# Optimization experiments

Measured on AMD Instinct MI355X. Metric: run time of the kernel, lower is better.

Reference implementation:

```python
import jax, jax.numpy as jnp
import numpy as np
import math

B, S, D, H, P = 4, 2048, 512, 8, 64
HD = D // H


def setup_inputs() -> dict:
    key = jax.random.key(0)
    ks = jax.random.split(key, 12)
    inp = {
        "query": jax.random.normal(ks[0], (B, S, D), jnp.float32),
        "key": jax.random.normal(ks[1], (B, S, D), jnp.float32),
        "value": jax.random.normal(ks[2], (B, S, D), jnp.float32),
        "query_pos_em": jax.random.normal(ks[3], (B, S, P), jnp.float32),
        "key_pos_em": jax.random.normal(ks[4], (B, S, P), jnp.float32),
        "mask": jax.random.randint(ks[5], (B, S), 0, 2, jnp.int32),
        # learned params (bias=False linears, LayerNorm affine)
        "Wq": jax.random.normal(ks[6], (D, D), jnp.float32) / math.sqrt(D),
        "Wk": jax.random.normal(ks[7], (D, D), jnp.float32) / math.sqrt(D),
        "Wv": jax.random.normal(ks[8], (D, D), jnp.float32) / math.sqrt(D),
        "Wo": jax.random.normal(ks[9], (D, D), jnp.float32) / math.sqrt(D),
        "ln_gamma": jnp.ones((D,), jnp.float32),
        "ln_beta": jnp.zeros((D,), jnp.float32),
    }
    return inp


def _split_heads(x):
    # (B,S,D) -> (B,H,S,HD)
    return x.reshape(B, S, H, HD).transpose(0, 2, 1, 3)


def reference(query, key, value, query_pos_em, key_pos_em, mask,
              Wq, Wk, Wv, Wo, ln_gamma, ln_beta):
    residual = query
    q = _split_heads(query @ Wq)
    k = _split_heads(key @ Wk)
    v = _split_heads(value @ Wv)

    # positional similarity: softmax over (B,S,S)
    simi = jax.nn.softmax(jnp.einsum('bqp,bkp->bqk', query_pos_em, key_pos_em), axis=-1)

    # scaled dot-product modulated elementwise by similarity (broadcast over heads)
    prod = jnp.einsum('bhqd,bhkd->bhqk', q, k) / math.sqrt(HD)
    prod = prod * simi[:, None, :, :]

    # additive mask: (mask-1)*1e8, broadcast [:, None, None, :]
    m = (mask.astype(prod.dtype) - 1.0) * 1e8
    prod = prod + m[:, None, None, :]

    attn = jax.nn.softmax(prod, axis=-1)
    out = jnp.einsum('bhqk,bhkd->bhqd', attn, v)  # (B,H,S,HD)
    out = out.transpose(0, 2, 1, 3).reshape(B, S, D)
    out = out @ Wo  # dropout is identity in eval mode

    x = residual + out
    mu = jnp.mean(x, axis=-1, keepdims=True)
    var = jnp.var(x, axis=-1, keepdims=True)
    return (x - mu) / jnp.sqrt(var + 1e-5) * ln_gamma + ln_beta
```

## Files before the change

kernel.cpp:

```cpp
#include <hip/hip_runtime.h>
#include <hip/hip_bf16.h>

#define Bq 4
#define Sq 2048
#define Dq 512
#define Hq 8
#define HDq 64
#define Pq 64

typedef __attribute__((ext_vector_type(8))) short short8;
typedef __attribute__((ext_vector_type(4))) float f32x4;

__device__ inline unsigned short f2bf(float f) {
  unsigned int u = __float_as_uint(f);
  unsigned int r = u + 0x7FFFu + ((u >> 16) & 1u);
  return (unsigned short)(r >> 16);
}
__device__ inline float bf2f(unsigned short s) {
  return __uint_as_float(((unsigned int)s) << 16);
}
__device__ inline short8 ld8f(const float* __restrict__ p) {
  const float4 a = *(const float4*)p;
  const float4 b = *(const float4*)(p + 4);
  short8 r;
  r[0] = (short)f2bf(a.x); r[1] = (short)f2bf(a.y); r[2] = (short)f2bf(a.z); r[3] = (short)f2bf(a.w);
  r[4] = (short)f2bf(b.x); r[5] = (short)f2bf(b.y); r[6] = (short)f2bf(b.z); r[7] = (short)f2bf(b.w);
  return r;
}

__global__ __launch_bounds__(256) void prep(const float* __restrict__ qpe,
                                            const float* __restrict__ kpe,
                                            const int* __restrict__ mask,
                                            unsigned short* __restrict__ qpeb,
                                            unsigned short* __restrict__ kpeb,
                                            float* __restrict__ mb) {
  const int bid = blockIdx.x;
  if (bid < 256) {
    int i = bid * 256 + threadIdx.x;
    *(short8*)&qpeb[(size_t)i * 8] = ld8f(qpe + (size_t)i * 8);
  } else if (bid < 512) {
    int i = (bid - 256) * 256 + threadIdx.x;
    *(short8*)&kpeb[(size_t)i * 8] = ld8f(kpe + (size_t)i * 8);
  } else {
    int i = (bid - 512) * 256 + threadIdx.x;
    mb[i] = ((float)mask[i] - 1.0f) * 1.442695041e8f;
  }
}

__global__ __launch_bounds__(256) void convW4(const float* __restrict__ Wq,
                                              const float* __restrict__ Wk,
                                              const float* __restrict__ Wv,
                                              const float* __restrict__ Wo,
                                              unsigned short* __restrict__ Wqt,
                                              unsigned short* __restrict__ Wkt,
                                              unsigned short* __restrict__ Wvt,
                                              unsigned short* __restrict__ Wot) {
  __shared__ float tile[32][33];
  const int z = blockIdx.z;
  const float* W = z == 0 ? Wq : z == 1 ? Wk : z == 2 ? Wv : Wo;
  unsigned short* Wt = z == 0 ? Wqt : z == 1 ? Wkt : z == 2 ? Wvt : Wot;
  const float scale = (z == 0) ? 0.125f : 1.0f;
  const int tx = threadIdx.x & 31, ty = threadIdx.x >> 5;
  const int n0 = blockIdx.x * 32, k0 = blockIdx.y * 32;
  for (int j = 0; j < 4; ++j)
    tile[ty + j * 8][tx] = W[(size_t)(k0 + ty + j * 8) * Dq + n0 + tx];
  __syncthreads();
  for (int j = 0; j < 4; ++j)
    Wt[(size_t)(n0 + ty + j * 8) * Dq + k0 + tx] = f2bf(tile[tx][ty + j * 8] * scale);
}

__global__ __launch_bounds__(256) void gemm_qkv(const float* __restrict__ Aq,
                                                const float* __restrict__ Ak,
                                                const float* __restrict__ Av,
                                                const unsigned short* __restrict__ Wqt,
                                                const unsigned short* __restrict__ Wkt,
                                                const unsigned short* __restrict__ Wvt,
                                                unsigned short* __restrict__ Qb,
                                                unsigned short* __restrict__ Kb,
                                                unsigned short* __restrict__ VbT) {
  __shared__ unsigned short Alds[64][72];
  __shared__ unsigned short Blds[64][72];
  const int z = blockIdx.z;
  const float* Ap = z == 0 ? Aq : z == 1 ? Ak : Av;
  const unsigned short* Wt = z == 0 ? Wqt : z == 1 ? Wkt : Wvt;
  unsigned short* Cb = z == 0 ? Qb : z == 1 ? Kb : VbT;
  const bool wt = (z == 2);
  const int tid = threadIdx.x;
  const int lane = tid & 63, wv = tid >> 6;
  const int wr = wv >> 1, wc = wv & 1;
  const int l15 = lane & 15, lg = lane >> 4;
  const int row0 = blockIdx.x * 64, col0 = blockIdx.y * 64;
  f32x4 acc[2][2] = {};
  for (int k0 = 0; k0 < Dq; k0 += 64) {
    __syncthreads();
    for (int h = 0; h < 2; ++h) {
      int id = tid + h * 256;
      int r = id >> 3, c8 = (id & 7) * 8;
      const float* ap = Ap + (size_t)(row0 + r) * Dq + k0 + c8;
      float4 f0 = *(const float4*)ap;
      float4 f1 = *(const float4*)(ap + 4);
      ushort4 u0 = {f2bf(f0.x), f2bf(f0.y), f2bf(f0.z), f2bf(f0.w)};
      ushort4 u1 = {f2bf(f1.x), f2bf(f1.y), f2bf(f1.z), f2bf(f1.w)};
      *(ushort4*)&Alds[r][c8] = u0;
      *(ushort4*)&Alds[r][c8 + 4] = u1;
      *(uint4*)&Blds[r][c8] = *(const uint4*)&Wt[(size_t)(col0 + r) * Dq + k0 + c8];
    }
    __syncthreads();
    short8 a[2][2], b[2][2];
    for (int mi = 0; mi < 2; ++mi)
      for (int kc = 0; kc < 2; ++kc)
        a[mi][kc] = *(const short8*)&Alds[wr * 32 + mi * 16 + l15][kc * 32 + lg * 8];
    for (int ni = 0; ni < 2; ++ni)
      for (int kc = 0; kc < 2; ++kc)
        b[ni][kc] = *(const short8*)&Blds[wc * 32 + ni * 16 + l15][kc * 32 + lg * 8];
    for (int mi = 0; mi < 2; ++mi)
      for (int ni = 0; ni < 2; ++ni) {
        acc[mi][ni] = __builtin_amdgcn_mfma_f32_16x16x32_bf16(a[mi][0], b[ni][0], acc[mi][ni], 0, 0, 0);
        acc[mi][ni] = __builtin_amdgcn_mfma_f32_16x16x32_bf16(a[mi][1], b[ni][1], acc[mi][ni], 0, 0, 0);
      }
  }
  const int orow = row0 + wr * 32 + lg * 4;
  const int ocol = col0 + wc * 32 + l15;
  if (wt) {
    const int bidx = orow >> 11;
    for (int mi = 0; mi < 2; ++mi)
      for (int ni = 0; ni < 2; ++ni) {
        int gc = ocol + ni * 16;
        int s = (orow + mi * 16) & (Sq - 1);
        ushort4 w = {f2bf(acc[mi][ni][0]), f2bf(acc[mi][ni][1]),
                     f2bf(acc[mi][ni][2]), f2bf(acc[mi][ni][3])};
        *(ushort4*)&Cb[((size_t)(bidx * Dq + gc)) * Sq + s] = w;
      }
  } else {
    for (int mi = 0; mi < 2; ++mi)
      for (int ni = 0; ni < 2; ++ni)
        for (int rr = 0; rr < 4; ++rr) {
          int gr = orow + mi * 16 + rr, gc = ocol + ni * 16;
          Cb[(size_t)gr * Dq + gc] = f2bf(acc[mi][ni][rr]);
        }
  }
}

__global__ __launch_bounds__(256) void gemm_wo(const unsigned short* __restrict__ Ab,
                                               const unsigned short* __restrict__ Wt,
                                               const float* __restrict__ res,
                                               float* __restrict__ Cf) {
  __shared__ unsigned short Alds[64][72];
  __shared__ unsigned short Blds[64][72];
  const int tid = threadIdx.x;
  const int lane = tid & 63, wv = tid >> 6;
  const int wr = wv >> 1, wc = wv & 1;
  const int l15 = lane & 15, lg = lane >> 4;
  const int row0 = blockIdx.x * 64, col0 = blockIdx.y * 64;
  f32x4 acc[2][2] = {};
  for (int k0 = 0; k0 < Dq; k0 += 64) {
    __syncthreads();
    for (int h = 0; h < 2; ++h) {
      int id = tid + h * 256;
      int r = id >> 3, c8 = (id & 7) * 8;
      *(uint4*)&Alds[r][c8] = *(const uint4*)&Ab[(size_t)(row0 + r) * Dq + k0 + c8];
      *(uint4*)&Blds[r][c8] = *(const uint4*)&Wt[(size_t)(col0 + r) * Dq + k0 + c8];
    }
    __syncthreads();
    short8 a[2][2], b[2][2];
    for (int mi = 0; mi < 2; ++mi)
      for (int kc = 0; kc < 2; ++kc)
        a[mi][kc] = *(const short8*)&Alds[wr * 32 + mi * 16 + l15][kc * 32 + lg * 8];
    for (int ni = 0; ni < 2; ++ni)
      for (int kc = 0; kc < 2; ++kc)
        b[ni][kc] = *(const short8*)&Blds[wc * 32 + ni * 16 + l15][kc * 32 + lg * 8];
    for (int mi = 0; mi < 2; ++mi)
      for (int ni = 0; ni < 2; ++ni) {
        acc[mi][ni] = __builtin_amdgcn_mfma_f32_16x16x32_bf16(a[mi][0], b[ni][0], acc[mi][ni], 0, 0, 0);
        acc[mi][ni] = __builtin_amdgcn_mfma_f32_16x16x32_bf16(a[mi][1], b[ni][1], acc[mi][ni], 0, 0, 0);
      }
  }
  const int orow = row0 + wr * 32 + lg * 4;
  const int ocol = col0 + wc * 32 + l15;
  for (int mi = 0; mi < 2; ++mi)
    for (int ni = 0; ni < 2; ++ni)
      for (int rr = 0; rr < 4; ++rr) {
        int gr = orow + mi * 16 + rr, gc = ocol + ni * 16;
        Cf[(size_t)gr * Dq + gc] = acc[mi][ni][rr] + res[(size_t)gr * Dq + gc];
      }
}

__global__ __launch_bounds__(256) void possim(const unsigned short* __restrict__ qpe,
                                              const unsigned short* __restrict__ kpe,
                                              unsigned short* __restrict__ simiB,
                                              float* __restrict__ invsum) {
  __shared__ float wsum[4][16];
  const int tid = threadIdx.x, lane = tid & 63, wv = tid >> 6;
  const int l15 = lane & 15, lg = lane >> 4;
  const int b = blockIdx.y, q0 = blockIdx.x * 16;
  const unsigned short* qrow = qpe + ((size_t)(b * Sq + q0 + l15)) * Pq + lg * 8;
  short8 aq0 = *(const short8*)qrow;
  short8 aq1 = *(const short8*)(qrow + 32);
  unsigned short* sB = simiB + ((size_t)(b * (Sq / 16) + blockIdx.x)) * Sq * 16;
  float lsum[4] = {0.f, 0.f, 0.f, 0.f};
  for (int t = wv; t < Sq / 64; t += 4) {
    int k0 = t * 64;
    f32x4 sc[4] = {};
#pragma unroll
    for (int ng = 0; ng < 4; ++ng) {
      const unsigned short* krow = kpe + ((size_t)(b * Sq + k0 + ng * 16 + l15)) * Pq + lg * 8;
      short8 bk0 = *(const short8*)krow;
      short8 bk1 = *(const short8*)(krow + 32);
      sc[ng] = __builtin_amdgcn_mfma_f32_16x16x32_bf16(aq0, bk0, sc[ng], 0, 0, 0);
      sc[ng] = __builtin_amdgcn_mfma_f32_16x16x32_bf16(aq1, bk1, sc[ng], 0, 0, 0);
    }
#pragma unroll
    for (int ng = 0; ng < 4; ++ng) {
      float e0 = __expf(sc[ng][0]);
      float e1 = __expf(sc[ng][1]);
      float e2 = __expf(sc[ng][2]);
      float e3 = __expf(sc[ng][3]);
      lsum[0] += e0; lsum[1] += e1; lsum[2] += e2; lsum[3] += e3;
      ushort4 st = {f2bf(e0), f2bf(e1), f2bf(e2), f2bf(e3)};
      *(ushort4*)&sB[(size_t)(k0 + ng * 16 + l15) * 16 + lg * 4] = st;
    }
  }
  for (int rr = 0; rr < 4; ++rr)
    for (int m = 1; m < 16; m <<= 1) lsum[rr] += __shfl_xor(lsum[rr], m, 64);
  if (l15 == 0)
    for (int rr = 0; rr < 4; ++rr) wsum[wv][lg * 4 + rr] = lsum[rr];
  __syncthreads();
  if (tid < 16) {
    float tot = wsum[0][tid] + wsum[1][tid] + wsum[2][tid] + wsum[3][tid];
    invsum[b * Sq + q0 + tid] = 1.0f / tot;
  }
}

__global__ __launch_bounds__(512) void attn(const unsigned short* __restrict__ Qb,
                                            const unsigned short* __restrict__ Kb,
                                            const unsigned short* __restrict__ VbT,
                                            const unsigned short* __restrict__ simiB,
                                            const float* __restrict__ invsum,
                                            const float* __restrict__ mbias,
                                            unsigned short* __restrict__ O) {
  __shared__ unsigned short Klds[2][64][72];
  __shared__ unsigned short Vlds[2][64][72];
  __shared__ unsigned short Plds[8][16][72];
  const int tid = threadIdx.x, lane = tid & 63, wv = tid >> 6;
  const int l15 = lane & 15, lg = lane >> 4;
  const int q0 = blockIdx.x * 128, h = blockIdx.y, b = blockIdx.z;
  const int qw = q0 + wv * 16;
  const int sr = tid >> 3, sc8 = (tid & 7) * 8;
  const unsigned short* Kg = Kb + ((size_t)(b * Sq + sr)) * Dq + h * HDq + sc8;
  const unsigned short* Vg = VbT + ((size_t)(b * Dq + h * HDq + sr)) * Sq + sc8;

  const unsigned short* qp = Qb + ((size_t)(b * Sq + qw + l15)) * Dq + h * HDq + lg * 8;
  short8 aq0 = *(const short8*)qp;
  short8 aq1 = *(const short8*)(qp + 32);
  float inv2[4];
#pragma unroll
  for (int rr = 0; rr < 4; ++rr)
    inv2[rr] = invsum[b * Sq + qw + lg * 4 + rr] * 1.442695041f;
  const unsigned short* sB =
      simiB + ((size_t)(b * (Sq / 16) + blockIdx.x * 8 + wv)) * Sq * 16 + lg * 4;
  const float* Mb = mbias + b * Sq;

  {
    *(uint4*)&Klds[0][sr][sc8] = *(const uint4*)Kg;
    *(uint4*)&Vlds[0][sr][sc8] = *(const uint4*)Vg;
  }
  f32x4 oacc[4] = {};
  float lsum[4] = {0.f, 0.f, 0.f, 0.f};
  int cur = 0;
  for (int t = 0; t < Sq / 64; ++t) {
    const int k0 = t * 64;
    __syncthreads();
    uint4 nk0, nv0;
    const bool more = (t < Sq / 64 - 1);
    if (more) {
      nk0 = *(const uint4*)(Kg + (size_t)(k0 + 64) * Dq);
      nv0 = *(const uint4*)(Vg + (k0 + 64));
    }
    ushort4 sv4[4];
    float mbf[4];
#pragma unroll
    for (int ng = 0; ng < 4; ++ng) {
      int kk = k0 + ng * 16 + l15;
      sv4[ng] = *(const ushort4*)&sB[(size_t)kk * 16];
      mbf[ng] = Mb[kk];
    }
    f32x4 sc[4] = {};
    __builtin_amdgcn_s_setprio(1);
#pragma unroll
    for (int ng = 0; ng < 4; ++ng) {
      short8 bk0 = *(const short8*)&Klds[cur][ng * 16 + l15][lg * 8];
      short8 bk1 = *(const short8*)&Klds[cur][ng * 16 + l15][32 + lg * 8];
      sc[ng] = __builtin_amdgcn_mfma_f32_16x16x32_bf16(aq0, bk0, sc[ng], 0, 0, 0);
      sc[ng] = __builtin_amdgcn_mfma_f32_16x16x32_bf16(aq1, bk1, sc[ng], 0, 0, 0);
    }
    __builtin_amdgcn_s_setprio(0);
#pragma unroll
    for (int ng = 0; ng < 4; ++ng) {
#pragma unroll
      for (int rr = 0; rr < 4; ++rr) {
        float sv = bf2f(rr == 0 ? sv4[ng].x : rr == 1 ? sv4[ng].y : rr == 2 ? sv4[ng].z
                                                                            : sv4[ng].w);
        float p = __builtin_amdgcn_exp2f(fmaf(sc[ng][rr] * sv, inv2[rr], mbf[ng]));
        lsum[rr] += p;
        Plds[wv][lg * 4 + rr][ng * 16 + l15] = f2bf(p);
      }
    }
    short8 pa0 = *(const short8*)&Plds[wv][l15][lg * 8];
    short8 pa1 = *(const short8*)&Plds[wv][l15][32 + lg * 8];
    __builtin_amdgcn_s_setprio(1);
#pragma unroll
    for (int dg = 0; dg < 4; ++dg) {
      short8 bv0 = *(const short8*)&Vlds[cur][dg * 16 + l15][lg * 8];
      short8 bv1 = *(const short8*)&Vlds[cur][dg * 16 + l15][32 + lg * 8];
      oacc[dg] = __builtin_amdgcn_mfma_f32_16x16x32_bf16(pa0, bv0, oacc[dg], 0, 0, 0);
      oacc[dg] = __builtin_amdgcn_mfma_f32_16x16x32_bf16(pa1, bv1, oacc[dg], 0, 0, 0);
    }
    __builtin_amdgcn_s_setprio(0);
    if (more) {
      *(uint4*)&Klds[cur ^ 1][sr][sc8] = nk0;
      *(uint4*)&Vlds[cur ^ 1][sr][sc8] = nv0;
      cur ^= 1;
    }
  }
#pragma unroll
  for (int rr = 0; rr < 4; ++rr)
    for (int m = 1; m < 16; m <<= 1) lsum[rr] += __shfl_xor(lsum[rr], m, 64);
#pragma unroll
  for (int dg = 0; dg < 4; ++dg)
    for (int rr = 0; rr < 4; ++rr) {
      int qg = qw + lg * 4 + rr;
      O[((size_t)(b * Sq + qg)) * Dq + h * HDq + dg * 16 + l15] = f2bf(oacc[dg][rr] / lsum[rr]);
    }
}

__global__ __launch_bounds__(256) void lnorm(float* __restrict__ X,
                                             const float* __restrict__ gamma,
                                             const float* __restrict__ beta) {
  const int tid = threadIdx.x, lane = tid & 63, wv = tid >> 6;
  const int row = blockIdx.x * 4 + wv;
  float* xr = X + (size_t)row * Dq + lane * 8;
  float4 x0 = *(float4*)xr;
  float4 x1 = *(float4*)(xr + 4);
  float s = x0.x + x0.y + x0.z + x0.w + x1.x + x1.y + x1.z + x1.w;
  float s2 = x0.x * x0.x + x0.y * x0.y + x0.z * x0.z + x0.w * x0.w +
             x1.x * x1.x + x1.y * x1.y + x1.z * x1.z + x1.w * x1.w;
  for (int m = 1; m < 64; m <<= 1) {
    s += __shfl_xor(s, m, 64);
    s2 += __shfl_xor(s2, m, 64);
  }
  float mu = s * (1.0f / 512.0f);
  float var = s2 * (1.0f / 512.0f) - mu * mu;
  float rstd = rsqrtf(var + 1e-5f);
  const float* g = gamma + lane * 8;
  const float* be = beta + lane * 8;
  float4 y0, y1;
  y0.x = (x0.x - mu) * rstd * g[0] + be[0];
  y0.y = (x0.y - mu) * rstd * g[1] + be[1];
  y0.z = (x0.z - mu) * rstd * g[2] + be[2];
  y0.w = (x0.w - mu) * rstd * g[3] + be[3];
  y1.x = (x1.x - mu) * rstd * g[4] + be[4];
  y1.y = (x1.y - mu) * rstd * g[5] + be[5];
  y1.z = (x1.z - mu) * rstd * g[6] + be[6];
  y1.w = (x1.w - mu) * rstd * g[7] + be[7];
  *(float4*)xr = y0;
  *(float4*)(xr + 4) = y1;
}

extern "C" void kernel_launch(void* const* d_in, const int* in_sizes, int n_in,
                              void* d_out, int out_size, void* d_ws, size_t ws_size,
                              hipStream_t stream) {
  const float* query = (const float*)d_in[0];
  const float* key = (const float*)d_in[1];
  const float* value = (const float*)d_in[2];
  const float* qpe = (const float*)d_in[3];
  const float* kpe = (const float*)d_in[4];
  const int* mask = (const int*)d_in[5];
  const float* Wq = (const float*)d_in[6];
  const float* Wk = (const float*)d_in[7];
  const float* Wv = (const float*)d_in[8];
  const float* Wo = (const float*)d_in[9];
  const float* gamma = (const float*)d_in[10];
  const float* beta = (const float*)d_in[11];
  float* out = (float*)d_out;

  char* ws = (char*)d_ws;
  size_t off = 0;
  unsigned short* Qb = (unsigned short*)(ws + off); off += (size_t)Bq * Sq * Dq * 2;
  unsigned short* Kb = (unsigned short*)(ws + off); off += (size_t)Bq * Sq * Dq * 2;
  unsigned short* VbT = (unsigned short*)(ws + off); off += (size_t)Bq * Sq * Dq * 2;
  unsigned short* Wqt = (unsigned short*)(ws + off); off += (size_t)Dq * Dq * 2;
  unsigned short* Wkt = (unsigned short*)(ws + off); off += (size_t)Dq * Dq * 2;
  unsigned short* Wvt = (unsigned short*)(ws + off); off += (size_t)Dq * Dq * 2;
  unsigned short* Wot = (unsigned short*)(ws + off); off += (size_t)Dq * Dq * 2;
  unsigned short* simiB = (unsigned short*)(ws + off); off += (size_t)Bq * Sq * Sq * 2;
  float* invsum = (float*)(ws + off); off += (size_t)Bq * Sq * 4;
  float* mbias = (float*)(ws + off); off += (size_t)Bq * Sq * 4;
  unsigned short* Ob = (unsigned short*)(ws + off); off += (size_t)Bq * Sq * Dq * 2;
  unsigned short* qpeb = (unsigned short*)(ws + off); off += (size_t)Bq * Sq * Pq * 2;
  unsigned short* kpeb = (unsigned short*)(ws + off); off += (size_t)Bq * Sq * Pq * 2;

  dim3 blk(256);
  prep<<<dim3(544), blk, 0, stream>>>(qpe, kpe, mask, qpeb, kpeb, mbias);
  convW4<<<dim3(16, 16, 4), blk, 0, stream>>>(Wq, Wk, Wv, Wo, Wqt, Wkt, Wvt, Wot);
  possim<<<dim3(Sq / 16, Bq), blk, 0, stream>>>(qpeb, kpeb, simiB, invsum);
  gemm_qkv<<<dim3(128, 8, 3), blk, 0, stream>>>(query, key, value, Wqt, Wkt, Wvt, Qb, Kb, VbT);
  attn<<<dim3(Sq / 128, Hq, Bq), dim3(512), 0, stream>>>(Qb, Kb, VbT, simiB, invsum, mbias, Ob);
  gemm_wo<<<dim3(128, 8), blk, 0, stream>>>(Ob, Wot, query, out);
  lnorm<<<dim3(Bq * Sq / 4), blk, 0, stream>>>(out, gamma, beta);
}
```

Baseline: 152.0 us.

## Enlarge GEMM tiles to 128x128 and swizzle attention P LDS layout

The QKV and output-projection GEMMs move from 64x64 to 128x128 block tiles, with each wave computing a 64x64 sub-tile (4x4 MFMA fragments). This raises data reuse per LDS load and cuts redundant global reads of A and W. The cost is more registers and fewer blocks (768 for QKV, 256 for Wo), which may leave the GPU underfilled. The attention kernel also XOR-swizzles the column index in the P scratch buffer in LDS to reduce bank conflicts on the transpose write/read.

```diff
diff --git a/kernel.cpp b/kernel.cpp
--- a/kernel.cpp
+++ b/kernel.cpp
@@ -78,8 +78,8 @@
                                                 unsigned short* __restrict__ Qb,
                                                 unsigned short* __restrict__ Kb,
                                                 unsigned short* __restrict__ VbT) {
-  __shared__ unsigned short Alds[64][72];
-  __shared__ unsigned short Blds[64][72];
+  __shared__ unsigned short Alds[128][72];
+  __shared__ unsigned short Blds[128][72];
   const int z = blockIdx.z;
   const float* Ap = z == 0 ? Aq : z == 1 ? Ak : Av;
   const unsigned short* Wt = z == 0 ? Wqt : z == 1 ? Wkt : Wvt;
@@ -89,42 +89,50 @@
   const int lane = tid & 63, wv = tid >> 6;
   const int wr = wv >> 1, wc = wv & 1;
   const int l15 = lane & 15, lg = lane >> 4;
-  const int row0 = blockIdx.x * 64, col0 = blockIdx.y * 64;
-  f32x4 acc[2][2] = {};
+  const int row0 = blockIdx.x * 128, col0 = blockIdx.y * 128;
+  f32x4 acc[4][4] = {};
   for (int k0 = 0; k0 < Dq; k0 += 64) {
     __syncthreads();
-    for (int h = 0; h < 2; ++h) {
-      int id = tid + h * 256;
-      int r = id >> 3, c8 = (id & 7) * 8;
+#pragma unroll
+    for (int j = 0; j < 4; ++j) {
+      int s = tid + j * 256;
+      int r = s >> 3, c8 = (s & 7) * 8;
       const float* ap = Ap + (size_t)(row0 + r) * Dq + k0 + c8;
       float4 f0 = *(const float4*)ap;
       float4 f1 = *(const float4*)(ap + 4);
-      ushort4 u0 = {f2bf(f0.x), f2bf(f0.y), f2bf(f0.z), f2bf(f0.w)};
-      ushort4 u1 = {f2bf(f1.x), f2bf(f1.y), f2bf(f1.z), f2bf(f1.w)};
-      *(ushort4*)&Alds[r][c8] = u0;
-      *(ushort4*)&Alds[r][c8 + 4] = u1;
+      short8 u;
+      u[0] = (short)f2bf(f0.x); u[1] = (short)f2bf(f0.y);
+      u[2] = (short)f2bf(f0.z); u[3] = (short)f2bf(f0.w);
+      u[4] = (short)f2bf(f1.x); u[5] = (short)f2bf(f1.y);
+      u[6] = (short)f2bf(f1.z); u[7] = (short)f2bf(f1.w);
+      *(short8*)&Alds[r][c8] = u;
       *(uint4*)&Blds[r][c8] = *(const uint4*)&Wt[(size_t)(col0 + r) * Dq + k0 + c8];
     }
     __syncthreads();
-    short8 a[2][2], b[2][2];
-    for (int mi = 0; mi < 2; ++mi)
-      for (int kc = 0; kc < 2; ++kc)
-        a[mi][kc] = *(const short8*)&Alds[wr * 32 + mi * 16 + l15][kc * 32 + lg * 8];
-    for (int ni = 0; ni < 2; ++ni)
-      for (int kc = 0; kc < 2; ++kc)
-        b[ni][kc] = *(const short8*)&Blds[wc * 32 + ni * 16 + l15][kc * 32 + lg * 8];
-    for (int mi = 0; mi < 2; ++mi)
-      for (int ni = 0; ni < 2; ++ni) {
-        acc[mi][ni] = __builtin_amdgcn_mfma_f32_16x16x32_bf16(a[mi][0], b[ni][0], acc[mi][ni], 0, 0, 0);
-        acc[mi][ni] = __builtin_amdgcn_mfma_f32_16x16x32_bf16(a[mi][1], b[ni][1], acc[mi][ni], 0, 0, 0);
-      }
-  }
-  const int orow = row0 + wr * 32 + lg * 4;
-  const int ocol = col0 + wc * 32 + l15;
+#pragma unroll
+    for (int kc = 0; kc < 2; ++kc) {
+      short8 a[4], b[4];
+#pragma unroll
+      for (int mi = 0; mi < 4; ++mi)
+        a[mi] = *(const short8*)&Alds[wr * 64 + mi * 16 + l15][kc * 32 + lg * 8];
+#pragma unroll
+      for (int ni = 0; ni < 4; ++ni)
+        b[ni] = *(const short8*)&Blds[wc * 64 + ni * 16 + l15][kc * 32 + lg * 8];
+#pragma unroll
+      for (int mi = 0; mi < 4; ++mi)
+#pragma unroll
+        for (int ni = 0; ni < 4; ++ni)
+          acc[mi][ni] = __builtin_amdgcn_mfma_f32_16x16x32_bf16(a[mi], b[ni], acc[mi][ni], 0, 0, 0);
+    }
+  }
+  const int orow = row0 + wr * 64 + lg * 4;
+  const int ocol = col0 + wc * 64 + l15;
   if (wt) {
     const int bidx = orow >> 11;
-    for (int mi = 0; mi < 2; ++mi)
-      for (int ni = 0; ni < 2; ++ni) {
+#pragma unroll
+    for (int mi = 0; mi < 4; ++mi)
+#pragma unroll
+      for (int ni = 0; ni < 4; ++ni) {
         int gc = ocol + ni * 16;
         int s = (orow + mi * 16) & (Sq - 1);
         ushort4 w = {f2bf(acc[mi][ni][0]), f2bf(acc[mi][ni][1]),
@@ -132,8 +140,11 @@
         *(ushort4*)&Cb[((size_t)(bidx * Dq + gc)) * Sq + s] = w;
       }
   } else {
-    for (int mi = 0; mi < 2; ++mi)
-      for (int ni = 0; ni < 2; ++ni)
+#pragma unroll
+    for (int mi = 0; mi < 4; ++mi)
+#pragma unroll
+      for (int ni = 0; ni < 4; ++ni)
+#pragma unroll
         for (int rr = 0; rr < 4; ++rr) {
           int gr = orow + mi * 16 + rr, gc = ocol + ni * 16;
           Cb[(size_t)gr * Dq + gc] = f2bf(acc[mi][ni][rr]);
@@ -145,40 +156,47 @@
                                                const unsigned short* __restrict__ Wt,
                                                const float* __restrict__ res,
                                                float* __restrict__ Cf) {
-  __shared__ unsigned short Alds[64][72];
-  __shared__ unsigned short Blds[64][72];
+  __shared__ unsigned short Alds[128][72];
+  __shared__ unsigned short Blds[128][72];
   const int tid = threadIdx.x;
   const int lane = tid & 63, wv = tid >> 6;
   const int wr = wv >> 1, wc = wv & 1;
   const int l15 = lane & 15, lg = lane >> 4;
-  const int row0 = blockIdx.x * 64, col0 = blockIdx.y * 64;
-  f32x4 acc[2][2] = {};
+  const int row0 = blockIdx.x * 128, col0 = blockIdx.y * 128;
+  f32x4 acc[4][4] = {};
   for (int k0 = 0; k0 < Dq; k0 += 64) {
     __syncthreads();
-    for (int h = 0; h < 2; ++h) {
-      int id = tid + h * 256;
-      int r = id >> 3, c8 = (id & 7) * 8;
+#pragma unroll
+    for (int j = 0; j < 4; ++j) {
+      int s = tid + j * 256;
+      int r = s >> 3, c8 = (s & 7) * 8;
       *(uint4*)&Alds[r][c8] = *(const uint4*)&Ab[(size_t)(row0 + r) * Dq + k0 + c8];
       *(uint4*)&Blds[r][c8] = *(const uint4*)&Wt[(size_t)(col0 + r) * Dq + k0 + c8];
     }
     __syncthreads();
-    short8 a[2][2], b[2][2];
-    for (int mi = 0; mi < 2; ++mi)
-      for (int kc = 0; kc < 2; ++kc)
-        a[mi][kc] = *(const short8*)&Alds[wr * 32 + mi * 16 + l15][kc * 32 + lg * 8];
-    for (int ni = 0; ni < 2; ++ni)
-      for (int kc = 0; kc < 2; ++kc)
-        b[ni][kc] = *(const short8*)&Blds[wc * 32 + ni * 16 + l15][kc * 32 + lg * 8];
-    for (int mi = 0; mi < 2; ++mi)
-      for (int ni = 0; ni < 2; ++ni) {
-        acc[mi][ni] = __builtin_amdgcn_mfma_f32_16x16x32_bf16(a[mi][0], b[ni][0], acc[mi][ni], 0, 0, 0);
-        acc[mi][ni] = __builtin_amdgcn_mfma_f32_16x16x32_bf16(a[mi][1], b[ni][1], acc[mi][ni], 0, 0, 0);
-      }
-  }
-  const int orow = row0 + wr * 32 + lg * 4;
-  const int ocol = col0 + wc * 32 + l15;
-  for (int mi = 0; mi < 2; ++mi)
-    for (int ni = 0; ni < 2; ++ni)
+#pragma unroll
+    for (int kc = 0; kc < 2; ++kc) {
+      short8 a[4], b[4];
+#pragma unroll
+      for (int mi = 0; mi < 4; ++mi)
+        a[mi] = *(const short8*)&Alds[wr * 64 + mi * 16 + l15][kc * 32 + lg * 8];
+#pragma unroll
+      for (int ni = 0; ni < 4; ++ni)
+        b[ni] = *(const short8*)&Blds[wc * 64 + ni * 16 + l15][kc * 32 + lg * 8];
+#pragma unroll
+      for (int mi = 0; mi < 4; ++mi)
+#pragma unroll
+        for (int ni = 0; ni < 4; ++ni)
+          acc[mi][ni] = __builtin_amdgcn_mfma_f32_16x16x32_bf16(a[mi], b[ni], acc[mi][ni], 0, 0, 0);
+    }
+  }
+  const int orow = row0 + wr * 64 + lg * 4;
+  const int ocol = col0 + wc * 64 + l15;
+#pragma unroll
+  for (int mi = 0; mi < 4; ++mi)
+#pragma unroll
+    for (int ni = 0; ni < 4; ++ni)
+#pragma unroll
       for (int rr = 0; rr < 4; ++rr) {
         int gr = orow + mi * 16 + rr, gc = ocol + ni * 16;
         Cf[(size_t)gr * Dq + gc] = acc[mi][ni][rr] + res[(size_t)gr * Dq + gc];
@@ -259,6 +277,8 @@
   const unsigned short* sB =
       simiB + ((size_t)(b * (Sq / 16) + blockIdx.x * 8 + wv)) * Sq * 16 + lg * 4;
   const float* Mb = mbias + b * Sq;
+  const int wxor = (lg >> 1) << 3;
+  const int lgs = lg ^ (l15 >> 3);
 
   {
     *(uint4*)&Klds[0][sr][sc8] = *(const uint4*)Kg;
@@ -302,11 +322,11 @@
                                                                             : sv4[ng].w);
         float p = __builtin_amdgcn_exp2f(fmaf(sc[ng][rr] * sv, inv2[rr], mbf[ng]));
         lsum[rr] += p;
-        Plds[wv][lg * 4 + rr][ng * 16 + l15] = f2bf(p);
+        Plds[wv][lg * 4 + rr][ng * 16 + (l15 ^ wxor)] = f2bf(p);
       }
     }
-    short8 pa0 = *(const short8*)&Plds[wv][l15][lg * 8];
-    short8 pa1 = *(const short8*)&Plds[wv][l15][32 + lg * 8];
+    short8 pa0 = *(const short8*)&Plds[wv][l15][lgs * 8];
+    short8 pa1 = *(const short8*)&Plds[wv][l15][32 + lgs * 8];
     __builtin_amdgcn_s_setprio(1);
 #pragma unroll
     for (int dg = 0; dg < 4; ++dg) {
@@ -403,8 +423,8 @@
   prep<<<dim3(544), blk, 0, stream>>>(qpe, kpe, mask, qpeb, kpeb, mbias);
   convW4<<<dim3(16, 16, 4), blk, 0, stream>>>(Wq, Wk, Wv, Wo, Wqt, Wkt, Wvt, Wot);
   possim<<<dim3(Sq / 16, Bq), blk, 0, stream>>>(qpeb, kpeb, simiB, invsum);
-  gemm_qkv<<<dim3(128, 8, 3), blk, 0, stream>>>(query, key, value, Wqt, Wkt, Wvt, Qb, Kb, VbT);
+  gemm_qkv<<<dim3(64, 4, 3), blk, 0, stream>>>(query, key, value, Wqt, Wkt, Wvt, Qb, Kb, VbT);
   attn<<<dim3(Sq / 128, Hq, Bq), dim3(512), 0, stream>>>(Qb, Kb, VbT, simiB, invsum, mbias, Ob);
-  gemm_wo<<<dim3(128, 8), blk, 0, stream>>>(Ob, Wot, query, out);
+  gemm_wo<<<dim3(64, 4), blk, 0, stream>>>(Ob, Wot, query, out);
   lnorm<<<dim3(Bq * Sq / 4), blk, 0, stream>>>(out, gamma, beta);
 }
```

New measurement: 149.1 us. No clear change (-1.9%).
